# Optimization experiments

Hardware: AMD Instinct MI355X
Metric: run time of the kernel (lower is better)

The kernel has to match this reference:

```python
import jax, jax.numpy as jnp
import numpy as np

EPS = 1e-12  # matches torch F.normalize default eps


def _l2_normalize(x):
    norm = jnp.linalg.norm(x, axis=-1, keepdims=True)
    return x / jnp.maximum(norm, EPS)


def setup_inputs() -> dict:
    key = jax.random.key(0)
    k1, k2 = jax.random.split(key)
    support = jax.random.normal(k1, (2, 5, 1024, 128), dtype=jnp.float32)
    query = jax.random.normal(k2, (2, 4, 1024, 128), dtype=jnp.float32)
    return {"support": support, "query": query}


def reference(support, query):
    # support: (b, j, n, k); query: (b, i, m, k)
    # cosine path: L2-normalize features then pairwise dot products.
    q = _l2_normalize(query)
    s = _l2_normalize(support)
    # output: (b, i, j, m, n)
    sim = jnp.einsum('bimk,bjnk->bijmn', q, s)
    return sim
```

## Files before the change

### kernel.cpp

```cpp
#include <hip/hip_runtime.h>
#include <stdint.h>


#define S_ROWS 10240
#define Q_ROWS 8192

typedef __attribute__((ext_vector_type(8))) short short8;
typedef __attribute__((ext_vector_type(4))) float floatx4;
typedef __attribute__((ext_vector_type(4))) unsigned int uint4x;

__device__ static inline unsigned short f32_to_bf16_rne(float f) {
    union { float f; uint32_t u; } c; c.f = f;
    uint32_t u = c.u;
    uint32_t r = u + 0x7FFFu + ((u >> 16) & 1u);
    return (unsigned short)(r >> 16);
}

__global__ __launch_bounds__(256) void norm_cast_kernel(
    const float* __restrict__ support, const float* __restrict__ query,
    unsigned short* __restrict__ sn, unsigned short* __restrict__ qn)
{
    int wave = blockIdx.x * 4 + (threadIdx.x >> 6);
    int lane = threadIdx.x & 63;

    const float* src;
    unsigned short* dst;
    if (wave < S_ROWS) {
        src = support + (size_t)wave * 128;
        dst = sn + (size_t)wave * 128;
    } else {
        int r = wave - S_ROWS;
        src = query + (size_t)r * 128;
        dst = qn + (size_t)r * 128;
    }

    float2 v = ((const float2*)src)[lane];
    float s = v.x * v.x + v.y * v.y;
    #pragma unroll
    for (int off = 32; off > 0; off >>= 1) s += __shfl_xor(s, off, 64);
    float inv = 1.0f / fmaxf(sqrtf(s), 1e-12f);

    unsigned short lo = f32_to_bf16_rne(v.x * inv);
    unsigned short hi = f32_to_bf16_rne(v.y * inv);
    ((uint32_t*)dst)[lane] = ((uint32_t)hi << 16) | (uint32_t)lo;
}

__global__ __launch_bounds__(256) void gemm_bt_kernel(
    const unsigned short* __restrict__ qn, const unsigned short* __restrict__ sn,
    float* __restrict__ out)
{
    __shared__ unsigned short As[128 * 128];
    __shared__ unsigned short Bs[128 * 128];

    const int tid  = threadIdx.x;
    const int wave = tid >> 6;
    const int lane = tid & 63;

    const int tn = blockIdx.x & 7;
    const int tm = blockIdx.x >> 3;
    const int y   = blockIdx.y;
    const int b   = y / 20;
    const int rem = y % 20;
    const int i   = rem / 5;
    const int j   = rem % 5;

    const unsigned short* gA = qn + (((size_t)(b * 4 + i) * 1024 + tm * 128) * 128);
    const unsigned short* gB = sn + (((size_t)(b * 5 + j) * 1024 + tn * 128) * 128);

    uint4x ra[8], rb[8];
    #pragma unroll
    for (int it = 0; it < 8; ++it) {
        ra[it] = ((const uint4x*)gA)[it * 256 + tid];
        rb[it] = ((const uint4x*)gB)[it * 256 + tid];
    }
    #pragma unroll
    for (int it = 0; it < 8; ++it) {
        const int u  = it * 256 + tid;
        const int r  = u >> 4;
        const int cl = u & 15;
        const int su = (r << 4) | (cl ^ (r & 15));
        *(uint4x*)&As[su * 8] = ra[it];
        *(uint4x*)&Bs[su * 8] = rb[it];
    }

    const int wm   = (wave >> 1) * 64;
    const int wn   = (wave & 1) * 64;
    const int ml   = lane & 15;
    const int quad = lane >> 4;

    floatx4 acc[4][4] = {};

    __syncthreads();

    #pragma unroll
    for (int kb = 0; kb < 4; ++kb) {
        const int c = kb * 4 + quad;
        short8 a[4], bf[4];
        #pragma unroll
        for (int mi = 0; mi < 4; ++mi) {
            const int arow = wm + mi * 16 + ml;
            a[mi] = *(const short8*)&As[(((arow << 4) | (c ^ ml))) * 8];
        }
        #pragma unroll
        for (int ni = 0; ni < 4; ++ni) {
            const int brow = wn + ni * 16 + ml;
            bf[ni] = *(const short8*)&Bs[(((brow << 4) | (c ^ ml))) * 8];
        }
        #pragma unroll
        for (int mi = 0; mi < 4; ++mi)
            #pragma unroll
            for (int ni = 0; ni < 4; ++ni)
                acc[mi][ni] = __builtin_amdgcn_mfma_f32_16x16x32_bf16(
                    a[mi], bf[ni], acc[mi][ni], 0, 0, 0);
    }

    float* gC = out + ((size_t)((b * 4 + i) * 5 + j) << 20)
                    + (size_t)(tm * 128) * 1024 + tn * 128;
    #pragma unroll
    for (int mi = 0; mi < 4; ++mi) {
        #pragma unroll
        for (int r = 0; r < 4; ++r) {
            const int row = wm + mi * 16 + quad * 4 + r;
            float* rowp = gC + (size_t)row * 1024 + wn + ml;
            #pragma unroll
            for (int ni = 0; ni < 4; ++ni)
                rowp[ni * 16] = acc[mi][ni][r];
        }
    }
}

extern "C" void kernel_launch(void* const* d_in, const int* in_sizes, int n_in,
                              void* d_out, int out_size, void* d_ws, size_t ws_size,
                              hipStream_t stream) {
    const float* support = (const float*)d_in[0];
    const float* query   = (const float*)d_in[1];
    unsigned short* sn = (unsigned short*)d_ws;
    unsigned short* qn = sn + (size_t)S_ROWS * 128;
    float* out = (float*)d_out;

    norm_cast_kernel<<<dim3((S_ROWS + Q_ROWS) / 4), dim3(256), 0, stream>>>(
        support, query, sn, qn);
    gemm_bt_kernel<<<dim3(64, 40), dim3(256), 0, stream>>>(qn, sn, out);
}
```

Measured before the change: 174.1 us.

## Keep query tile in registers and stream double-buffered support tiles

Each block now loads its 128-row query tile once into registers and loops over ten 64-row support tiles (all five j sets for two n-tiles). The support tiles are double-buffered in shared memory, with register prefetch two tiles ahead. This cuts redundant A-tile loads and overlaps B loading with compute, while the grid shrinks from 2560 to 512 persistent-style blocks. The kernel is dominated by the 160 MiB fp32 output write, so the main risk is fewer blocks reducing store parallelism, plus higher register pressure at launch_bounds(256,2).

```diff
diff --git a/kernel.cpp b/kernel.cpp
--- a/kernel.cpp
+++ b/kernel.cpp
@@ -45,86 +45,113 @@
     ((uint32_t*)dst)[lane] = ((uint32_t)hi << 16) | (uint32_t)lo;
 }
 
-__global__ __launch_bounds__(256) void gemm_bt_kernel(
+__global__ __launch_bounds__(256, 2) void gemm_bt_kernel(
     const unsigned short* __restrict__ qn, const unsigned short* __restrict__ sn,
     float* __restrict__ out)
 {
-    __shared__ unsigned short As[128 * 128];
-    __shared__ unsigned short Bs[128 * 128];
+    __shared__ unsigned short Bs[2][64 * 128];
 
     const int tid  = threadIdx.x;
     const int wave = tid >> 6;
     const int lane = tid & 63;
 
-    const int tn = blockIdx.x & 7;
-    const int tm = blockIdx.x >> 3;
-    const int y   = blockIdx.y;
-    const int b   = y / 20;
-    const int rem = y % 20;
-    const int i   = rem / 5;
-    const int j   = rem % 5;
+    const int x  = blockIdx.x;
+    const int bi = x & 7;
+    const int tm = (x >> 3) & 7;
+    const int q  = x >> 6;
+    const int b  = bi >> 2;
 
-    const unsigned short* gA = qn + (((size_t)(b * 4 + i) * 1024 + tm * 128) * 128);
-    const unsigned short* gB = sn + (((size_t)(b * 5 + j) * 1024 + tn * 128) * 128);
+    const int wm   = (wave >> 1) * 64;
+    const int wn   = (wave & 1) * 32;
+    const int ml   = lane & 15;
+    const int quad = lane >> 4;
 
-    uint4x ra[8], rb[8];
+    const unsigned short* gA = qn + ((size_t)bi * 1024 + tm * 128) * 128;
+    short8 a[4][4];
     #pragma unroll
-    for (int it = 0; it < 8; ++it) {
-        ra[it] = ((const uint4x*)gA)[it * 256 + tid];
-        rb[it] = ((const uint4x*)gB)[it * 256 + tid];
+    for (int kb = 0; kb < 4; ++kb)
+        #pragma unroll
+        for (int mi = 0; mi < 4; ++mi)
+            a[kb][mi] = *(const short8*)&gA[
+                (size_t)(wm + mi * 16 + ml) * 128 + (kb * 4 + quad) * 8];
+
+    const unsigned short* sb = sn + (size_t)b * 5 * 1024 * 128;
+    const uint4x* bp[10];
+    #pragma unroll
+    for (int t = 0; t < 10; ++t) {
+        const int j  = t >> 1;
+        const int tn = q * 2 + (t & 1);
+        bp[t] = (const uint4x*)(sb + ((size_t)j * 1024 + tn * 64) * 128);
     }
+
+    uint4x rb[2][4];
     #pragma unroll
-    for (int it = 0; it < 8; ++it) {
+    for (int it = 0; it < 4; ++it) rb[0][it] = bp[0][it * 256 + tid];
+    #pragma unroll
+    for (int it = 0; it < 4; ++it) rb[1][it] = bp[1][it * 256 + tid];
+
+    #pragma unroll
+    for (int it = 0; it < 4; ++it) {
         const int u  = it * 256 + tid;
         const int r  = u >> 4;
         const int cl = u & 15;
         const int su = (r << 4) | (cl ^ (r & 15));
-        *(uint4x*)&As[su * 8] = ra[it];
-        *(uint4x*)&Bs[su * 8] = rb[it];
+        *(uint4x*)&Bs[0][su * 8] = rb[0][it];
     }
 
-    const int wm   = (wave >> 1) * 64;
-    const int wn   = (wave & 1) * 64;
-    const int ml   = lane & 15;
-    const int quad = lane >> 4;
-
-    floatx4 acc[4][4] = {};
-
-    __syncthreads();
+    float* gC0 = out + ((size_t)(bi * 5) << 20) + (size_t)(tm * 128) * 1024;
 
     #pragma unroll
-    for (int kb = 0; kb < 4; ++kb) {
-        const int c = kb * 4 + quad;
-        short8 a[4], bf[4];
+    for (int t = 0; t < 10; ++t) {
+        __syncthreads();
+
+        if (t < 9) {
+            #pragma unroll
+            for (int it = 0; it < 4; ++it) {
+                const int u  = it * 256 + tid;
+                const int r  = u >> 4;
+                const int cl = u & 15;
+                const int su = (r << 4) | (cl ^ (r & 15));
+                *(uint4x*)&Bs[(t + 1) & 1][su * 8] = rb[(t + 1) & 1][it];
+            }
+        }
+        if (t < 8) {
+            #pragma unroll
+            for (int it = 0; it < 4; ++it)
+                rb[t & 1][it] = bp[t + 2][it * 256 + tid];
+        }
+
+        floatx4 acc[4][2] = {};
+        #pragma unroll
+        for (int kb = 0; kb < 4; ++kb) {
+            const int c = kb * 4 + quad;
+            short8 bf[2];
+            #pragma unroll
+            for (int ni = 0; ni < 2; ++ni) {
+                const int brow = wn + ni * 16 + ml;
+                bf[ni] = *(const short8*)&Bs[t & 1][((brow << 4) | (c ^ ml)) * 8];
+            }
+            #pragma unroll
+            for (int mi = 0; mi < 4; ++mi)
+                #pragma unroll
+                for (int ni = 0; ni < 2; ++ni)
+                    acc[mi][ni] = __builtin_amdgcn_mfma_f32_16x16x32_bf16(
+                        a[kb][mi], bf[ni], acc[mi][ni], 0, 0, 0);
+        }
+
+        const int j  = t >> 1;
+        const int tn = q * 2 + (t & 1);
+        float* gC = gC0 + ((size_t)j << 20) + tn * 64;
         #pragma unroll
         for (int mi = 0; mi < 4; ++mi) {
-            const int arow = wm + mi * 16 + ml;
-            a[mi] = *(const short8*)&As[(((arow << 4) | (c ^ ml))) * 8];
-        }
-        #pragma unroll
-        for (int ni = 0; ni < 4; ++ni) {
-            const int brow = wn + ni * 16 + ml;
-            bf[ni] = *(const short8*)&Bs[(((brow << 4) | (c ^ ml))) * 8];
-        }
-        #pragma unroll
-        for (int mi = 0; mi < 4; ++mi)
             #pragma unroll
-            for (int ni = 0; ni < 4; ++ni)
-                acc[mi][ni] = __builtin_amdgcn_mfma_f32_16x16x32_bf16(
-                    a[mi], bf[ni], acc[mi][ni], 0, 0, 0);
-    }
-
-    float* gC = out + ((size_t)((b * 4 + i) * 5 + j) << 20)
-                    + (size_t)(tm * 128) * 1024 + tn * 128;
-    #pragma unroll
-    for (int mi = 0; mi < 4; ++mi) {
-        #pragma unroll
-        for (int r = 0; r < 4; ++r) {
-            const int row = wm + mi * 16 + quad * 4 + r;
-            float* rowp = gC + (size_t)row * 1024 + wn + ml;
-            #pragma unroll
-            for (int ni = 0; ni < 4; ++ni)
-                rowp[ni * 16] = acc[mi][ni][r];
+            for (int r = 0; r < 4; ++r) {
+                const int row = wm + mi * 16 + quad * 4 + r;
+                float* rowp = gC + (size_t)row * 1024 + wn + ml;
+                #pragma unroll
+                for (int ni = 0; ni < 2; ++ni)
+                    rowp[ni * 16] = acc[mi][ni][r];
+            }
         }
     }
 }
@@ -140,5 +167,5 @@
 
     norm_cast_kernel<<<dim3((S_ROWS + Q_ROWS) / 4), dim3(256), 0, stream>>>(
         support, query, sn, qn);
-    gemm_bt_kernel<<<dim3(64, 40), dim3(256), 0, stream>>>(qn, sn, out);
+    gemm_bt_kernel<<<dim3(512), dim3(256), 0, stream>>>(qn, sn, out);
 }
```

Result: no change. 176.4 us (+1.3%).
